# Kernel optimization log

Measured on AMD Instinct MI355X. Metric: run time of the kernel, lower is better.

Reference implementation:

```python
import jax, jax.numpy as jnp
import numpy as np

B, T, D, H = 4, 1024, 512, 8
DH = D // H
MLP = 4 * D
EPS = 1e-6


def _clinear(xr, xi, Wr, Wi, br, bi):
    # Naive complex Linear = two real nn.Linear layers (each adds its own bias):
    # re = Lr(xr) - Li(xi), im = Lr(xi) + Li(xr)
    re = xr @ Wr.T - xi @ Wi.T + (br - bi)
    im = xi @ Wr.T + xr @ Wi.T + (br + bi)
    return re, im


def _cln(xr, xi):
    # NaiveComplexLayerNorm: real LayerNorm (no affine) on re and im separately
    def ln(v):
        m = jnp.mean(v, -1, keepdims=True)
        va = jnp.var(v, -1, keepdims=True)
        return (v - m) * jax.lax.rsqrt(va + EPS)
    return ln(xr), ln(xi)


def _modulate(xr, xi, shr, shi, scr, sci):
    # complex x * (1 + scale) + shift, scale/shift are [B,D] broadcast over seq
    a, b = (1.0 + scr)[:, None, :], sci[:, None, :]
    return xr * a - xi * b + shr[:, None, :], xr * b + xi * a + shi[:, None, :]


def _gate(gr, gi, xr, xi):
    a, b = gr[:, None, :], gi[:, None, :]
    return xr * a - xi * b, xr * b + xi * a


def _heads(x):  # [B,T,D] -> [B,H,T,DH]
    return x.reshape(B, T, H, DH).transpose(0, 2, 1, 3)


def reference(x_re, x_im, c_re, c_im,
              ada_Wr, ada_Wi, ada_br, ada_bi,
              q_Wr, q_Wi, q_br, q_bi,
              k_Wr, k_Wi, k_br, k_bi,
              v_Wr, v_Wi, v_br, v_bi,
              o_Wr, o_Wi, o_br, o_bi,
              f1_Wr, f1_Wi, f1_br, f1_bi,
              f2_Wr, f2_Wi, f2_br, f2_bi):
    # adaLN_modulation: complex SiLU -> complex Linear -> 6 chunks along dim 1
    sr, si = jax.nn.silu(c_re), jax.nn.silu(c_im)
    mr, mi = _clinear(sr, si, ada_Wr, ada_Wi, ada_br, ada_bi)
    sh_ar, sc_ar, g_ar, sh_mr, sc_mr, g_mr = jnp.split(mr, 6, axis=1)
    sh_ai, sc_ai, g_ai, sh_mi, sc_mi, g_mi = jnp.split(mi, 6, axis=1)

    nr, ni = _cln(x_re, x_im)
    hr, hi = _modulate(nr, ni, sh_ar, sh_ai, sc_ar, sc_ai)

    qr, qi = _clinear(hr, hi, q_Wr, q_Wi, q_br, q_bi)
    kr, ki = _clinear(hr, hi, k_Wr, k_Wi, k_br, k_bi)
    vr, vi = _clinear(hr, hi, v_Wr, v_Wi, v_br, v_bi)
    qr, qi, kr, ki, vr, vi = map(_heads, (qr, qi, kr, ki, vr, vi))

    scale = 1.0 / jnp.sqrt(jnp.float32(DH))
    # complex scores q @ k^T (no conjugation, matching plain complex matmul)
    s_re = (jnp.einsum('bhqd,bhkd->bhqk', qr, kr) - jnp.einsum('bhqd,bhkd->bhqk', qi, ki)) * scale
    s_im = (jnp.einsum('bhqd,bhkd->bhqk', qr, ki) + jnp.einsum('bhqd,bhkd->bhqk', qi, kr)) * scale
    # naive complex softmax: real softmax applied to re/im independently
    a_re = jax.nn.softmax(s_re, axis=-1)
    a_im = jax.nn.softmax(s_im, axis=-1)
    o_r = jnp.einsum('bhqk,bhkd->bhqd', a_re, vr) - jnp.einsum('bhqk,bhkd->bhqd', a_im, vi)
    o_i = jnp.einsum('bhqk,bhkd->bhqd', a_re, vi) + jnp.einsum('bhqk,bhkd->bhqd', a_im, vr)
    o_r = o_r.transpose(0, 2, 1, 3).reshape(B, T, D)
    o_i = o_i.transpose(0, 2, 1, 3).reshape(B, T, D)
    o_r, o_i = _clinear(o_r, o_i, o_Wr, o_Wi, o_br, o_bi)

    gr, gi = _gate(g_ar, g_ai, o_r, o_i)
    x_re, x_im = x_re + gr, x_im + gi

    # ---- MLP branch
    nr, ni = _cln(x_re, x_im)
    hr, hi = _modulate(nr, ni, sh_mr, sh_mi, sc_mr, sc_mi)
    hr, hi = _clinear(hr, hi, f1_Wr, f1_Wi, f1_br, f1_bi)
    hr = jax.nn.gelu(hr, approximate=True)  # ComplexGELU(tanh) per component
    hi = jax.nn.gelu(hi, approximate=True)
    hr, hi = _clinear(hr, hi, f2_Wr, f2_Wi, f2_br, f2_bi)
    gr, gi = _gate(g_mr, g_mi, hr, hi)
    return jnp.stack([x_re + gr, x_im + gi])  # [2,B,T,D] = (real, imag)


def setup_inputs() -> dict:
    key = jax.random.key(0)
    ks = iter(jax.random.split(key, 48))

    def rn(shape, s=1.0):
        return jax.random.normal(next(ks), shape, dtype=jnp.float32) * s

    inp = {'x_re': rn((B, T, D)), 'x_im': rn((B, T, D)),
           'c_re': rn((B, D)), 'c_im': rn((B, D))}

    def lin(name, din, dout):
        inp[name + '_Wr'] = rn((dout, din), 0.02)
        inp[name + '_Wi'] = rn((dout, din), 0.02)
        inp[name + '_br'] = rn((dout,), 0.02)
        inp[name + '_bi'] = rn((dout,), 0.02)

    lin('ada', D, 6 * D)
    for n in ('q', 'k', 'v', 'o'):
        lin(n, D, D)
    lin('f1', D, MLP)
    lin('f2', MLP, D)
    return inp
```

## Files before the change

### kernel.cpp

```cpp
#include <hip/hip_runtime.h>


typedef unsigned short u16;
typedef __attribute__((ext_vector_type(8))) __bf16 bf16x8;
typedef __attribute__((ext_vector_type(8))) u16    u16x8;
typedef __attribute__((ext_vector_type(4))) u16    u16x4;
typedef __attribute__((ext_vector_type(4))) float  f32x4;

#define MFMA16(a, b, c) __builtin_amdgcn_mfma_f32_16x16x32_bf16(a, b, c, 0, 0, 0)

static constexpr int Bd = 4, Td = 1024, Dd = 512, Hd = 8, DHd = 64, MLPd = 2048;

__device__ __forceinline__ u16 f2bf(float x) {
  return __builtin_bit_cast(u16, (__bf16)x);
}
__device__ __forceinline__ bf16x8 ldsfrag(const u16* p) {
  return __builtin_bit_cast(bf16x8, *(const u16x8*)p);
}
__device__ __forceinline__ bf16x8 negbf(bf16x8 v) {
  u16x8 u = __builtin_bit_cast(u16x8, v);
  u ^= (u16)0x8000;
  return __builtin_bit_cast(bf16x8, u);
}
__device__ __forceinline__ float gelu_tanh(float x) {
  float t = tanhf(0.7978845608028654f * (x + 0.044715f * x * x * x));
  return 0.5f * x * (1.f + t);
}

struct CJobs {
  const float* src[12];
  u16* dst[12];
  int blk_start[13];
};
__global__ __launch_bounds__(256) void convert_kernel(CJobs J) {
  const int blk = blockIdx.x;
  int jj = 0;
  while (jj < 11 && blk >= J.blk_start[jj + 1]) ++jj;
  const int idx = (blk - J.blk_start[jj]) * 256 + threadIdx.x;
  const float4 v = ((const float4*)J.src[jj])[idx];
  u16x4 o;
  o[0] = f2bf(v.x); o[1] = f2bf(v.y); o[2] = f2bf(v.z); o[3] = f2bf(v.w);
  *(u16x4*)(J.dst[jj] + (size_t)idx * 4) = o;
}

__global__ __launch_bounds__(256) void ada_kernel(
    const float* __restrict__ c_re, const float* __restrict__ c_im,
    const float* __restrict__ Wr, const float* __restrict__ Wi,
    const float* __restrict__ br, const float* __restrict__ bi,
    float* __restrict__ m_r, float* __restrict__ m_i) {
  __shared__ __align__(16) float sr[512], si[512];
  const int b = blockIdx.x / 12, nb = blockIdx.x % 12;
  const int tid = threadIdx.x;
  for (int i = tid; i < 512; i += 256) {
    const float xr = c_re[b * 512 + i], xi = c_im[b * 512 + i];
    sr[i] = xr / (1.f + __expf(-xr));
    si[i] = xi / (1.f + __expf(-xi));
  }
  __syncthreads();
  const int n = nb * 256 + tid;
  const float4* wr4 = (const float4*)(Wr + (size_t)n * 512);
  const float4* wi4 = (const float4*)(Wi + (size_t)n * 512);
  const float4* sr4 = (const float4*)sr;
  const float4* si4 = (const float4*)si;
  float ar = 0.f, ai = 0.f;
  for (int k = 0; k < 128; ++k) {
    const float4 a_ = sr4[k], b_ = si4[k], u = wr4[k], v = wi4[k];
    ar += a_.x * u.x - b_.x * v.x + a_.y * u.y - b_.y * v.y +
          a_.z * u.z - b_.z * v.z + a_.w * u.w - b_.w * v.w;
    ai += b_.x * u.x + a_.x * v.x + b_.y * u.y + a_.y * v.y +
          b_.z * u.z + a_.z * v.z + b_.w * u.w + a_.w * v.w;
  }
  m_r[(size_t)b * 3072 + n] = ar + br[n] - bi[n];
  m_i[(size_t)b * 3072 + n] = ai + br[n] + bi[n];
}

__global__ __launch_bounds__(256) void ln_mod_kernel(
    const float* __restrict__ xr, const float* __restrict__ xi,
    const float* __restrict__ mv_r, const float* __restrict__ mv_i,
    int off_sh, int off_sc,
    u16* __restrict__ hr, u16* __restrict__ hi) {
  const int row = blockIdx.x;
  const int b = row >> 10;
  const int tid = threadIdx.x;
  const float* xrp = xr + (size_t)row * 512;
  const float* xip = xi + (size_t)row * 512;
  const float r0 = xrp[tid], r1 = xrp[tid + 256];
  const float i0 = xip[tid], i1 = xip[tid + 256];
  float s0 = r0 + r1, s1 = r0 * r0 + r1 * r1;
  float s2 = i0 + i1, s3 = i0 * i0 + i1 * i1;
  #pragma unroll
  for (int o = 32; o > 0; o >>= 1) {
    s0 += __shfl_down(s0, o); s1 += __shfl_down(s1, o);
    s2 += __shfl_down(s2, o); s3 += __shfl_down(s3, o);
  }
  __shared__ float red[4][4];
  if ((tid & 63) == 0) {
    const int wv = tid >> 6;
    red[wv][0] = s0; red[wv][1] = s1; red[wv][2] = s2; red[wv][3] = s3;
  }
  __syncthreads();
  s0 = red[0][0] + red[1][0] + red[2][0] + red[3][0];
  s1 = red[0][1] + red[1][1] + red[2][1] + red[3][1];
  s2 = red[0][2] + red[1][2] + red[2][2] + red[3][2];
  s3 = red[0][3] + red[1][3] + red[2][3] + red[3][3];
  const float mr = s0 * (1.f / 512.f), mi = s2 * (1.f / 512.f);
  const float vr = s1 * (1.f / 512.f) - mr * mr;
  const float vi = s3 * (1.f / 512.f) - mi * mi;
  const float rr = rsqrtf(vr + 1e-6f), ri = rsqrtf(vi + 1e-6f);
  const float* shr = mv_r + (size_t)b * 3072 + off_sh;
  const float* shi = mv_i + (size_t)b * 3072 + off_sh;
  const float* scr = mv_r + (size_t)b * 3072 + off_sc;
  const float* sci = mv_i + (size_t)b * 3072 + off_sc;
  #pragma unroll
  for (int jj = 0; jj < 2; ++jj) {
    const int n = tid + jj * 256;
    const float nr = ((jj ? r1 : r0) - mr) * rr;
    const float ni = ((jj ? i1 : i0) - mi) * ri;
    const float a = 1.f + scr[n], bb = sci[n];
    hr[(size_t)row * 512 + n] = f2bf(nr * a - ni * bb + shr[n]);
    hi[(size_t)row * 512 + n] = f2bf(nr * bb + ni * a + shi[n]);
  }
}

template <int EPI>
__global__ __launch_bounds__(256) void cgemm_kernel(
    const u16* __restrict__ Ar, const u16* __restrict__ Ai,
    const u16* __restrict__ W0r, const u16* __restrict__ W0i,
    const float* __restrict__ b0r, const float* __restrict__ b0i,
    const u16* __restrict__ W1r, const u16* __restrict__ W1i,
    const float* __restrict__ b1r, const float* __restrict__ b1i,
    const u16* __restrict__ W2r, const u16* __restrict__ W2i,
    const float* __restrict__ b2r, const float* __restrict__ b2i,
    int K, int ntiles_per_seg, int out_ld,
    u16* __restrict__ o0r, u16* __restrict__ o0i,
    u16* __restrict__ o1r, u16* __restrict__ o1i,
    u16* __restrict__ o2r, u16* __restrict__ o2i,
    const float* __restrict__ resid_r, const float* __restrict__ resid_i,
    const float* __restrict__ gate_r, const float* __restrict__ gate_i,
    float* __restrict__ ofr, float* __restrict__ ofi) {
  const int seg = blockIdx.y / ntiles_per_seg;
  const int n0 = (blockIdx.y % ntiles_per_seg) * 64;
  const int m0 = blockIdx.x * 64;
  const u16* Wr = (seg == 0) ? W0r : (seg == 1) ? W1r : W2r;
  const u16* Wi = (seg == 0) ? W0i : (seg == 1) ? W1i : W2i;
  const float* br = (seg == 0) ? b0r : (seg == 1) ? b1r : b2r;
  const float* bi = (seg == 0) ? b0i : (seg == 1) ? b1i : b2i;
  u16* obr = (seg == 0) ? o0r : (seg == 1) ? o1r : o2r;
  u16* obi = (seg == 0) ? o0i : (seg == 1) ? o1i : o2i;

  __shared__ __align__(16) u16 sA[2][64 * 72];
  __shared__ __align__(16) u16 sB[2][64 * 72];

  const int tid = threadIdx.x;
  const int w = tid >> 6, lane = tid & 63;
  const int wm = w >> 1, wn = w & 1;
  const int q4 = lane >> 4, c = lane & 15;

  const f32x4 z = {0.f, 0.f, 0.f, 0.f};
  f32x4 accR[2][2], accI[2][2];
  for (int a = 0; a < 2; ++a)
    for (int b2 = 0; b2 < 2; ++b2) { accR[a][b2] = z; accI[a][b2] = z; }

  for (int kt = 0; kt < K; kt += 64) {
    for (int idx = tid; idx < 512; idx += 256) {
      const int row = idx >> 3, cg = idx & 7;
      const int lo = row * 72 + cg * 8;
      *(u16x8*)&sA[0][lo] = *(const u16x8*)(Ar + (size_t)(m0 + row) * K + kt + cg * 8);
      *(u16x8*)&sA[1][lo] = *(const u16x8*)(Ai + (size_t)(m0 + row) * K + kt + cg * 8);
      *(u16x8*)&sB[0][lo] = *(const u16x8*)(Wr + (size_t)(n0 + row) * K + kt + cg * 8);
      *(u16x8*)&sB[1][lo] = *(const u16x8*)(Wi + (size_t)(n0 + row) * K + kt + cg * 8);
    }
    __syncthreads();
    #pragma unroll
    for (int kc = 0; kc < 2; ++kc) {
      bf16x8 a_r[2], a_i[2], a_n[2];
      #pragma unroll
      for (int mi = 0; mi < 2; ++mi) {
        const int off = (wm * 32 + mi * 16 + c) * 72 + kc * 32 + q4 * 8;
        a_r[mi] = ldsfrag(&sA[0][off]);
        a_i[mi] = ldsfrag(&sA[1][off]);
        a_n[mi] = negbf(a_i[mi]);
      }
      #pragma unroll
      for (int ni = 0; ni < 2; ++ni) {
        const int off = (wn * 32 + ni * 16 + c) * 72 + kc * 32 + q4 * 8;
        const bf16x8 b_r = ldsfrag(&sB[0][off]);
        const bf16x8 b_i = ldsfrag(&sB[1][off]);
        #pragma unroll
        for (int mi = 0; mi < 2; ++mi) {
          accR[mi][ni] = MFMA16(a_r[mi], b_r, accR[mi][ni]);
          accR[mi][ni] = MFMA16(a_n[mi], b_i, accR[mi][ni]);
          accI[mi][ni] = MFMA16(a_i[mi], b_r, accI[mi][ni]);
          accI[mi][ni] = MFMA16(a_r[mi], b_i, accI[mi][ni]);
        }
      }
    }
    __syncthreads();
  }

  const float scale = (EPI == 0 && seg == 0) ? 0.125f : 1.f;
  #pragma unroll
  for (int mi = 0; mi < 2; ++mi)
    #pragma unroll
    for (int ni = 0; ni < 2; ++ni) {
      const int n = n0 + wn * 32 + ni * 16 + c;
      const float biasr = br[n] - bi[n];
      const float biasi = br[n] + bi[n];
      if (EPI == 0 && seg == 2) {
        const int m = m0 + wm * 32 + mi * 16 + q4 * 4;
        u16x4 pr, pi;
        #pragma unroll
        for (int r = 0; r < 4; ++r) {
          pr[r] = f2bf(accR[mi][ni][r] + biasr);
          pi[r] = f2bf(accI[mi][ni][r] + biasi);
        }
        const size_t o = ((size_t)((m >> 10) * 512 + n)) * 1024 + (m & 1023);
        *(u16x4*)(obr + o) = pr;
        *(u16x4*)(obi + o) = pi;
        continue;
      }
      #pragma unroll
      for (int r = 0; r < 4; ++r) {
        const int m = m0 + wm * 32 + mi * 16 + q4 * 4 + r;
        const float ore = accR[mi][ni][r] + biasr;
        const float oim = accI[mi][ni][r] + biasi;
        if (EPI == 0) {
          obr[(size_t)m * out_ld + n] = f2bf(ore * scale);
          obi[(size_t)m * out_ld + n] = f2bf(oim * scale);
        } else if (EPI == 2) {
          obr[(size_t)m * out_ld + n] = f2bf(gelu_tanh(ore));
          obi[(size_t)m * out_ld + n] = f2bf(gelu_tanh(oim));
        } else {
          const int bb = m >> 10;
          const float gr = gate_r[(size_t)bb * 3072 + n];
          const float gi = gate_i[(size_t)bb * 3072 + n];
          const size_t o = (size_t)m * 512 + n;
          ofr[o] = resid_r[o] + ore * gr - oim * gi;
          ofi[o] = resid_i[o] + ore * gi + oim * gr;
        }
      }
    }
}

__global__ __launch_bounds__(256) void attn_kernel(
    const u16* __restrict__ Qr, const u16* __restrict__ Qi,
    const u16* __restrict__ Kr, const u16* __restrict__ Ki,
    const u16* __restrict__ Vtr, const u16* __restrict__ Vti,
    u16* __restrict__ Or, u16* __restrict__ Oi) {
  __shared__ __align__(16) u16 sK[2][64 * 72];
  __shared__ __align__(16) u16 sV[2][64 * 72];

  const int tid = threadIdx.x;
  const int w = tid >> 6, lane = tid & 63;
  const int q4 = lane >> 4, c = lane & 15;
  const int bh = blockIdx.y, b = bh >> 3, h = bh & 7;
  const int t0 = blockIdx.x * 64;
  const size_t base = (size_t)b * Td * Dd + h * DHd;
  const size_t vbase = (size_t)bh << 16;

  bf16x8 aQr[2], aQi[2], aQn[2];
  #pragma unroll
  for (int kc = 0; kc < 2; ++kc) {
    const size_t g = base + (size_t)(t0 + w * 16 + c) * Dd + kc * 32 + q4 * 8;
    aQr[kc] = __builtin_bit_cast(bf16x8, *(const u16x8*)(Qr + g));
    aQi[kc] = __builtin_bit_cast(bf16x8, *(const u16x8*)(Qi + g));
    aQn[kc] = negbf(aQi[kc]);
  }

  float mst[2][4], lst[2][4];
  #pragma unroll
  for (int p = 0; p < 2; ++p)
    for (int r = 0; r < 4; ++r) { mst[p][r] = -1e30f; lst[p][r] = 0.f; }
  const f32x4 z = {0.f, 0.f, 0.f, 0.f};
  f32x4 U1[4], U2[4], U3[4], U4[4];
  for (int i = 0; i < 4; ++i) { U1[i] = z; U2[i] = z; U3[i] = z; U4[i] = z; }

  const int srow = tid >> 3, scg = tid & 7;
  u16x8 R[2][4];
  #pragma unroll
  for (int it = 0; it < 2; ++it) {
    const int row = srow + it * 32;
    const size_t gk = base + (size_t)row * Dd + scg * 8;
    const size_t gv = vbase + (size_t)row * Td + scg * 8;
    R[it][0] = *(const u16x8*)(Kr + gk);
    R[it][1] = *(const u16x8*)(Ki + gk);
    R[it][2] = *(const u16x8*)(Vtr + gv);
    R[it][3] = *(const u16x8*)(Vti + gv);
  }

  for (int kt = 0; kt < 16; ++kt) {
    __syncthreads();
    #pragma unroll
    for (int it = 0; it < 2; ++it) {
      const int lo = (srow + it * 32) * 72 + scg * 8;
      *(u16x8*)&sK[0][lo] = R[it][0];
      *(u16x8*)&sK[1][lo] = R[it][1];
      *(u16x8*)&sV[0][lo] = R[it][2];
      *(u16x8*)&sV[1][lo] = R[it][3];
    }
    if (kt < 15) {
      #pragma unroll
      for (int it = 0; it < 2; ++it) {
        const int row = srow + it * 32;
        const size_t gk = base + (size_t)((kt + 1) * 64 + row) * Dd + scg * 8;
        const size_t gv = vbase + (size_t)row * Td + (kt + 1) * 64 + scg * 8;
        R[it][0] = *(const u16x8*)(Kr + gk);
        R[it][1] = *(const u16x8*)(Ki + gk);
        R[it][2] = *(const u16x8*)(Vtr + gv);
        R[it][3] = *(const u16x8*)(Vti + gv);
      }
    }
    __syncthreads();

    f32x4 S[2][4];
    __builtin_amdgcn_s_setprio(1);
    #pragma unroll
    for (int nb = 0; nb < 4; ++nb) {
      f32x4 tr = z, ti = z;
      #pragma unroll
      for (int kc = 0; kc < 2; ++kc) {
        const int off = (nb * 16 + c) * 72 + kc * 32 + q4 * 8;
        const bf16x8 bKr = ldsfrag(&sK[0][off]);
        const bf16x8 bKi = ldsfrag(&sK[1][off]);
        tr = MFMA16(aQr[kc], bKr, tr);
        tr = MFMA16(aQn[kc], bKi, tr);
        ti = MFMA16(aQi[kc], bKr, ti);
        ti = MFMA16(aQr[kc], bKi, ti);
      }
      S[0][nb] = tr; S[1][nb] = ti;
    }
    __builtin_amdgcn_s_setprio(0);
    __syncthreads();

    float alpha[2][4];
    #pragma unroll
    for (int p = 0; p < 2; ++p) {
      float rs[4];
      #pragma unroll
      for (int r = 0; r < 4; ++r) {
        float tm = fmaxf(fmaxf(S[p][0][r], S[p][1][r]), fmaxf(S[p][2][r], S[p][3][r]));
        #pragma unroll
        for (int o = 1; o < 16; o <<= 1) tm = fmaxf(tm, __shfl_xor(tm, o));
        const float mn = fmaxf(mst[p][r], tm);
        alpha[p][r] = __expf(mst[p][r] - mn);
        mst[p][r] = mn;
        rs[r] = 0.f;
      }
      #pragma unroll
      for (int nb = 0; nb < 4; ++nb)
        #pragma unroll
        for (int r = 0; r < 4; ++r) {
          const float pv = __expf(S[p][nb][r] - mst[p][r]);
          rs[r] += pv;
          sK[p][(w * 16 + q4 * 4 + r) * 72 + nb * 16 + c] = f2bf(pv);
        }
      #pragma unroll
      for (int r = 0; r < 4; ++r) {
        float s = rs[r];
        #pragma unroll
        for (int o = 1; o < 16; o <<= 1) s += __shfl_xor(s, o);
        lst[p][r] = lst[p][r] * alpha[p][r] + s;
      }
    }
    #pragma unroll
    for (int i = 0; i < 4; ++i)
      #pragma unroll
      for (int r = 0; r < 4; ++r) {
        U1[i][r] *= alpha[0][r]; U2[i][r] *= alpha[0][r];
        U3[i][r] *= alpha[1][r]; U4[i][r] *= alpha[1][r];
      }
    asm volatile("s_waitcnt lgkmcnt(0)" ::: "memory");
    __builtin_amdgcn_s_setprio(1);
    #pragma unroll
    for (int kc = 0; kc < 2; ++kc) {
      const int poff = (w * 16 + c) * 72 + kc * 32 + q4 * 8;
      const bf16x8 aPr = ldsfrag(&sK[0][poff]);
      const bf16x8 aPi = ldsfrag(&sK[1][poff]);
      #pragma unroll
      for (int nd = 0; nd < 4; ++nd) {
        const int voff = (nd * 16 + c) * 72 + kc * 32 + q4 * 8;
        const bf16x8 bVr = ldsfrag(&sV[0][voff]);
        const bf16x8 bVi = ldsfrag(&sV[1][voff]);
        U1[nd] = MFMA16(aPr, bVr, U1[nd]);
        U2[nd] = MFMA16(aPr, bVi, U2[nd]);
        U3[nd] = MFMA16(aPi, bVr, U3[nd]);
        U4[nd] = MFMA16(aPi, bVi, U4[nd]);
      }
    }
    __builtin_amdgcn_s_setprio(0);
  }

  #pragma unroll
  for (int nd = 0; nd < 4; ++nd)
    #pragma unroll
    for (int r = 0; r < 4; ++r) {
      const int trow = t0 + w * 16 + q4 * 4 + r;
      const int d = nd * 16 + c;
      const float ilre = 1.f / lst[0][r], ilim = 1.f / lst[1][r];
      const float ore = U1[nd][r] * ilre - U4[nd][r] * ilim;
      const float oim = U2[nd][r] * ilre + U3[nd][r] * ilim;
      const size_t g = base + (size_t)trow * Dd + d;
      Or[g] = f2bf(ore);
      Oi[g] = f2bf(oim);
    }
}

extern "C" void kernel_launch(void* const* d_in, const int* in_sizes, int n_in,
                              void* d_out, int out_size, void* d_ws, size_t ws_size,
                              hipStream_t stream) {
  const float* x_re  = (const float*)d_in[0];
  const float* x_im  = (const float*)d_in[1];
  const float* c_re  = (const float*)d_in[2];
  const float* c_im  = (const float*)d_in[3];
  const float* adaWr = (const float*)d_in[4];
  const float* adaWi = (const float*)d_in[5];
  const float* adabr = (const float*)d_in[6];
  const float* adabi = (const float*)d_in[7];
  const float* qWr = (const float*)d_in[8],  *qWi = (const float*)d_in[9];
  const float* qbr = (const float*)d_in[10], *qbi = (const float*)d_in[11];
  const float* kWr = (const float*)d_in[12], *kWi = (const float*)d_in[13];
  const float* kbr = (const float*)d_in[14], *kbi = (const float*)d_in[15];
  const float* vWr = (const float*)d_in[16], *vWi = (const float*)d_in[17];
  const float* vbr = (const float*)d_in[18], *vbi = (const float*)d_in[19];
  const float* oWr = (const float*)d_in[20], *oWi = (const float*)d_in[21];
  const float* obr = (const float*)d_in[22], *obi = (const float*)d_in[23];
  const float* f1Wr = (const float*)d_in[24], *f1Wi = (const float*)d_in[25];
  const float* f1br = (const float*)d_in[26], *f1bi = (const float*)d_in[27];
  const float* f2Wr = (const float*)d_in[28], *f2Wi = (const float*)d_in[29];
  const float* f2br = (const float*)d_in[30], *f2bi = (const float*)d_in[31];

  char* wsp = (char*)d_ws;
  size_t off = 0;
  auto alloc = [&](size_t bytes) -> void* {
    void* p = wsp + off;
    off += (bytes + 255) & ~(size_t)255;
    return p;
  };
  const size_t WQ = 512 * 512, WF = 2048 * 512;
  u16* wqr = (u16*)alloc(WQ * 2); u16* wqi = (u16*)alloc(WQ * 2);
  u16* wkr = (u16*)alloc(WQ * 2); u16* wki = (u16*)alloc(WQ * 2);
  u16* wvr = (u16*)alloc(WQ * 2); u16* wvi = (u16*)alloc(WQ * 2);
  u16* wor = (u16*)alloc(WQ * 2); u16* woi = (u16*)alloc(WQ * 2);
  u16* wf1r = (u16*)alloc(WF * 2); u16* wf1i = (u16*)alloc(WF * 2);
  u16* wf2r = (u16*)alloc(WF * 2); u16* wf2i = (u16*)alloc(WF * 2);
  float* m_r = (float*)alloc(4 * 3072 * 4);
  float* m_i = (float*)alloc(4 * 3072 * 4);
  const size_t ACT = (size_t)Bd * Td * Dd;
  u16* h1r = (u16*)alloc(ACT * 2); u16* h1i = (u16*)alloc(ACT * 2);
  u16* qbr_ = (u16*)alloc(ACT * 2); u16* qbi_ = (u16*)alloc(ACT * 2);
  u16* kbr_ = (u16*)alloc(ACT * 2); u16* kbi_ = (u16*)alloc(ACT * 2);
  u16* vbr_ = (u16*)alloc(ACT * 2); u16* vbi_ = (u16*)alloc(ACT * 2);
  u16* atr = (u16*)alloc(ACT * 2); u16* ati = (u16*)alloc(ACT * 2);
  float* x2r = (float*)alloc(ACT * 4); float* x2i = (float*)alloc(ACT * 4);
  u16* h2r = h1r; u16* h2i = h1i;
  u16* f1or = qbr_;
  u16* f1oi = qbr_ + (size_t)Bd * Td * MLPd;

  CJobs J;
  const float* wsrc[12] = {qWr, qWi, kWr, kWi, vWr, vWi, oWr, oWi, f1Wr, f1Wi, f2Wr, f2Wi};
  u16* wdst[12] = {wqr, wqi, wkr, wki, wvr, wvi, wor, woi, wf1r, wf1i, wf2r, wf2i};
  int cum = 0;
  for (int j = 0; j < 12; ++j) {
    J.src[j] = wsrc[j]; J.dst[j] = wdst[j]; J.blk_start[j] = cum;
    cum += (j < 8 ? (int)WQ : (int)WF) / 1024;
  }
  J.blk_start[12] = cum;
  convert_kernel<<<cum, 256, 0, stream>>>(J);

  ada_kernel<<<48, 256, 0, stream>>>(c_re, c_im, adaWr, adaWi, adabr, adabi, m_r, m_i);

  ln_mod_kernel<<<4096, 256, 0, stream>>>(x_re, x_im, m_r, m_i, 0, 512, h1r, h1i);

  cgemm_kernel<0><<<dim3(64, 24), 256, 0, stream>>>(
      h1r, h1i, wqr, wqi, qbr, qbi, wkr, wki, kbr, kbi, wvr, wvi, vbr, vbi,
      512, 8, 512, qbr_, qbi_, kbr_, kbi_, vbr_, vbi_,
      nullptr, nullptr, nullptr, nullptr, nullptr, nullptr);

  attn_kernel<<<dim3(16, 32), 256, 0, stream>>>(qbr_, qbi_, kbr_, kbi_, vbr_, vbi_, atr, ati);

  cgemm_kernel<1><<<dim3(64, 8), 256, 0, stream>>>(
      atr, ati, wor, woi, obr, obi, wor, woi, obr, obi, wor, woi, obr, obi,
      512, 8, 512, nullptr, nullptr, nullptr, nullptr, nullptr, nullptr,
      x_re, x_im, m_r + 1024, m_i + 1024, x2r, x2i);

  ln_mod_kernel<<<4096, 256, 0, stream>>>(x2r, x2i, m_r, m_i, 1536, 2048, h2r, h2i);

  cgemm_kernel<2><<<dim3(64, 32), 256, 0, stream>>>(
      h2r, h2i, wf1r, wf1i, f1br, f1bi, wf1r, wf1i, f1br, f1bi, wf1r, wf1i, f1br, f1bi,
      512, 32, 2048, f1or, f1oi, nullptr, nullptr, nullptr, nullptr,
      nullptr, nullptr, nullptr, nullptr, nullptr, nullptr);

  float* outp = (float*)d_out;
  cgemm_kernel<3><<<dim3(64, 8), 256, 0, stream>>>(
      f1or, f1oi, wf2r, wf2i, f2br, f2bi, wf2r, wf2i, f2br, f2bi, wf2r, wf2i, f2br, f2bi,
      2048, 8, 512, nullptr, nullptr, nullptr, nullptr, nullptr, nullptr,
      x2r, x2i, m_r + 2560, m_i + 2560, outp, outp + ACT);
}
```

Measured before the change: 460.9 us.

## Load attention K/V fragments directly from global, use DPP reductions and exp2

The attention kernel drops the shared K/V staging and its block-wide barriers. Each wave now loads its K and V MFMA fragments straight from global memory (relying on cache reuse across waves) and keeps only a small per-wave shared buffer for P. Row max and sum reductions use DPP row-rotate instead of shuffles, and softmax uses exp2, with log2(e) folded into the Q scale. Launch bounds request 2 blocks per CU. The trade-off is four times more global/L2 fragment traffic per block with no register prefetch, against fewer syncs and less LDS traffic.

Result: slower. 478.0 us (+3.7%).

```diff
diff --git a/kernel.cpp b/kernel.cpp
--- a/kernel.cpp
+++ b/kernel.cpp
@@ -14,7 +14,13 @@
 __device__ __forceinline__ u16 f2bf(float x) {
   return __builtin_bit_cast(u16, (__bf16)x);
 }
+__device__ __forceinline__ float exp2fast(float x) {
+  return __builtin_amdgcn_exp2f(x);
+}
 __device__ __forceinline__ bf16x8 ldsfrag(const u16* p) {
+  return __builtin_bit_cast(bf16x8, *(const u16x8*)p);
+}
+__device__ __forceinline__ bf16x8 gfrag(const u16* p) {
   return __builtin_bit_cast(bf16x8, *(const u16x8*)p);
 }
 __device__ __forceinline__ bf16x8 negbf(bf16x8 v) {
@@ -25,6 +31,27 @@
 __device__ __forceinline__ float gelu_tanh(float x) {
   float t = tanhf(0.7978845608028654f * (x + 0.044715f * x * x * x));
   return 0.5f * x * (1.f + t);
+}
+
+template <int CTRL>
+__device__ __forceinline__ float dppror(float x) {
+  const int xi = __builtin_bit_cast(int, x);
+  return __builtin_bit_cast(float,
+      __builtin_amdgcn_update_dpp(xi, xi, CTRL, 0xf, 0xf, false));
+}
+__device__ __forceinline__ float red16max(float x) {
+  x = fmaxf(x, dppror<0x128>(x));
+  x = fmaxf(x, dppror<0x124>(x));
+  x = fmaxf(x, dppror<0x122>(x));
+  x = fmaxf(x, dppror<0x121>(x));
+  return x;
+}
+__device__ __forceinline__ float red16sum(float x) {
+  x += dppror<0x128>(x);
+  x += dppror<0x124>(x);
+  x += dppror<0x122>(x);
+  x += dppror<0x121>(x);
+  return x;
 }
 
 struct CJobs {
@@ -198,7 +225,7 @@
     __syncthreads();
   }
 
-  const float scale = (EPI == 0 && seg == 0) ? 0.125f : 1.f;
+  const float scale = (EPI == 0 && seg == 0) ? 0.18033688011112042f : 1.f;
   #pragma unroll
   for (int mi = 0; mi < 2; ++mi)
     #pragma unroll
@@ -242,13 +269,12 @@
     }
 }
 
-__global__ __launch_bounds__(256) void attn_kernel(
+__global__ __launch_bounds__(256, 2) void attn_kernel(
     const u16* __restrict__ Qr, const u16* __restrict__ Qi,
     const u16* __restrict__ Kr, const u16* __restrict__ Ki,
     const u16* __restrict__ Vtr, const u16* __restrict__ Vti,
     u16* __restrict__ Or, u16* __restrict__ Oi) {
-  __shared__ __align__(16) u16 sK[2][64 * 72];
-  __shared__ __align__(16) u16 sV[2][64 * 72];
+  __shared__ __align__(16) u16 sP[2][4][16 * 72];
 
   const int tid = threadIdx.x;
   const int w = tid >> 6, lane = tid & 63;
@@ -262,8 +288,8 @@
   #pragma unroll
   for (int kc = 0; kc < 2; ++kc) {
     const size_t g = base + (size_t)(t0 + w * 16 + c) * Dd + kc * 32 + q4 * 8;
-    aQr[kc] = __builtin_bit_cast(bf16x8, *(const u16x8*)(Qr + g));
-    aQi[kc] = __builtin_bit_cast(bf16x8, *(const u16x8*)(Qi + g));
+    aQr[kc] = gfrag(Qr + g);
+    aQi[kc] = gfrag(Qi + g);
     aQn[kc] = negbf(aQi[kc]);
   }
 
@@ -275,42 +301,19 @@
   f32x4 U1[4], U2[4], U3[4], U4[4];
   for (int i = 0; i < 4; ++i) { U1[i] = z; U2[i] = z; U3[i] = z; U4[i] = z; }
 
-  const int srow = tid >> 3, scg = tid & 7;
-  u16x8 R[2][4];
-  #pragma unroll
-  for (int it = 0; it < 2; ++it) {
-    const int row = srow + it * 32;
-    const size_t gk = base + (size_t)row * Dd + scg * 8;
-    const size_t gv = vbase + (size_t)row * Td + scg * 8;
-    R[it][0] = *(const u16x8*)(Kr + gk);
-    R[it][1] = *(const u16x8*)(Ki + gk);
-    R[it][2] = *(const u16x8*)(Vtr + gv);
-    R[it][3] = *(const u16x8*)(Vti + gv);
-  }
+  u16* const pR = &sP[0][w][0];
+  u16* const pI = &sP[1][w][0];
 
   for (int kt = 0; kt < 16; ++kt) {
-    __syncthreads();
-    #pragma unroll
-    for (int it = 0; it < 2; ++it) {
-      const int lo = (srow + it * 32) * 72 + scg * 8;
-      *(u16x8*)&sK[0][lo] = R[it][0];
-      *(u16x8*)&sK[1][lo] = R[it][1];
-      *(u16x8*)&sV[0][lo] = R[it][2];
-      *(u16x8*)&sV[1][lo] = R[it][3];
-    }
-    if (kt < 15) {
-      #pragma unroll
-      for (int it = 0; it < 2; ++it) {
-        const int row = srow + it * 32;
-        const size_t gk = base + (size_t)((kt + 1) * 64 + row) * Dd + scg * 8;
-        const size_t gv = vbase + (size_t)row * Td + (kt + 1) * 64 + scg * 8;
-        R[it][0] = *(const u16x8*)(Kr + gk);
-        R[it][1] = *(const u16x8*)(Ki + gk);
-        R[it][2] = *(const u16x8*)(Vtr + gv);
-        R[it][3] = *(const u16x8*)(Vti + gv);
-      }
-    }
-    __syncthreads();
+    bf16x8 kR[4][2], kI[4][2];
+    #pragma unroll
+    for (int nb = 0; nb < 4; ++nb)
+      #pragma unroll
+      for (int kc = 0; kc < 2; ++kc) {
+        const size_t g = base + (size_t)(kt * 64 + nb * 16 + c) * Dd + kc * 32 + q4 * 8;
+        kR[nb][kc] = gfrag(Kr + g);
+        kI[nb][kc] = gfrag(Ki + g);
+      }
 
     f32x4 S[2][4];
     __builtin_amdgcn_s_setprio(1);
@@ -319,30 +322,36 @@
       f32x4 tr = z, ti = z;
       #pragma unroll
       for (int kc = 0; kc < 2; ++kc) {
-        const int off = (nb * 16 + c) * 72 + kc * 32 + q4 * 8;
-        const bf16x8 bKr = ldsfrag(&sK[0][off]);
-        const bf16x8 bKi = ldsfrag(&sK[1][off]);
-        tr = MFMA16(aQr[kc], bKr, tr);
-        tr = MFMA16(aQn[kc], bKi, tr);
-        ti = MFMA16(aQi[kc], bKr, ti);
-        ti = MFMA16(aQr[kc], bKi, ti);
+        tr = MFMA16(aQr[kc], kR[nb][kc], tr);
+        tr = MFMA16(aQn[kc], kI[nb][kc], tr);
+        ti = MFMA16(aQi[kc], kR[nb][kc], ti);
+        ti = MFMA16(aQr[kc], kI[nb][kc], ti);
       }
       S[0][nb] = tr; S[1][nb] = ti;
     }
     __builtin_amdgcn_s_setprio(0);
-    __syncthreads();
+
+    bf16x8 vR[4][2], vI[4][2];
+    #pragma unroll
+    for (int nd = 0; nd < 4; ++nd)
+      #pragma unroll
+      for (int kc = 0; kc < 2; ++kc) {
+        const size_t gv = vbase + (size_t)(nd * 16 + c) * Td + kt * 64 + kc * 32 + q4 * 8;
+        vR[nd][kc] = gfrag(Vtr + gv);
+        vI[nd][kc] = gfrag(Vti + gv);
+      }
 
     float alpha[2][4];
     #pragma unroll
     for (int p = 0; p < 2; ++p) {
+      u16* const pp = (p == 0) ? pR : pI;
       float rs[4];
       #pragma unroll
       for (int r = 0; r < 4; ++r) {
         float tm = fmaxf(fmaxf(S[p][0][r], S[p][1][r]), fmaxf(S[p][2][r], S[p][3][r]));
-        #pragma unroll
-        for (int o = 1; o < 16; o <<= 1) tm = fmaxf(tm, __shfl_xor(tm, o));
+        tm = red16max(tm);
         const float mn = fmaxf(mst[p][r], tm);
-        alpha[p][r] = __expf(mst[p][r] - mn);
+        alpha[p][r] = exp2fast(mst[p][r] - mn);
         mst[p][r] = mn;
         rs[r] = 0.f;
       }
@@ -350,17 +359,13 @@
       for (int nb = 0; nb < 4; ++nb)
         #pragma unroll
         for (int r = 0; r < 4; ++r) {
-          const float pv = __expf(S[p][nb][r] - mst[p][r]);
+          const float pv = exp2fast(S[p][nb][r] - mst[p][r]);
           rs[r] += pv;
-          sK[p][(w * 16 + q4 * 4 + r) * 72 + nb * 16 + c] = f2bf(pv);
+          pp[(q4 * 4 + r) * 72 + nb * 16 + c] = f2bf(pv);
         }
       #pragma unroll
-      for (int r = 0; r < 4; ++r) {
-        float s = rs[r];
-        #pragma unroll
-        for (int o = 1; o < 16; o <<= 1) s += __shfl_xor(s, o);
-        lst[p][r] = lst[p][r] * alpha[p][r] + s;
-      }
+      for (int r = 0; r < 4; ++r)
+        lst[p][r] = lst[p][r] * alpha[p][r] + red16sum(rs[r]);
     }
     #pragma unroll
     for (int i = 0; i < 4; ++i)
@@ -369,22 +374,20 @@
         U1[i][r] *= alpha[0][r]; U2[i][r] *= alpha[0][r];
         U3[i][r] *= alpha[1][r]; U4[i][r] *= alpha[1][r];
       }
+
     asm volatile("s_waitcnt lgkmcnt(0)" ::: "memory");
     __builtin_amdgcn_s_setprio(1);
     #pragma unroll
     for (int kc = 0; kc < 2; ++kc) {
-      const int poff = (w * 16 + c) * 72 + kc * 32 + q4 * 8;
-      const bf16x8 aPr = ldsfrag(&sK[0][poff]);
-      const bf16x8 aPi = ldsfrag(&sK[1][poff]);
+      const int poff = c * 72 + kc * 32 + q4 * 8;
+      const bf16x8 aPr = ldsfrag(pR + poff);
+      const bf16x8 aPi = ldsfrag(pI + poff);
       #pragma unroll
       for (int nd = 0; nd < 4; ++nd) {
-        const int voff = (nd * 16 + c) * 72 + kc * 32 + q4 * 8;
-        const bf16x8 bVr = ldsfrag(&sV[0][voff]);
-        const bf16x8 bVi = ldsfrag(&sV[1][voff]);
-        U1[nd] = MFMA16(aPr, bVr, U1[nd]);
-        U2[nd] = MFMA16(aPr, bVi, U2[nd]);
-        U3[nd] = MFMA16(aPi, bVr, U3[nd]);
-        U4[nd] = MFMA16(aPi, bVi, U4[nd]);
+        U1[nd] = MFMA16(aPr, vR[nd][kc], U1[nd]);
+        U2[nd] = MFMA16(aPr, vI[nd][kc], U2[nd]);
+        U3[nd] = MFMA16(aPi, vR[nd][kc], U3[nd]);
+        U4[nd] = MFMA16(aPi, vI[nd][kc], U4[nd]);
       }
     }
     __builtin_amdgcn_s_setprio(0);
```
